# Optimization experiments

Measured on AMD Instinct MI355X. Metric: run time of the kernel, lower is better.

The kernel has to match this reference:

```python
import jax, jax.numpy as jnp
import numpy as np

B, N, F_IN, H, S = 8, 2048, 128, 128, 2
ALPHA = 0.1  # LeakyReLU slope


def setup_inputs() -> dict:
    key = jax.random.key(0)
    ks = jax.random.split(key, 10)
    X_bt = jax.random.normal(ks[0], (B, N, F_IN), dtype=jnp.float32)
    distance_matrix = jax.random.uniform(ks[1], (N, N), dtype=jnp.float32)
    sigmas = jnp.array([0.2, 1.0], dtype=jnp.float32)  # GaussianKernelGenerator scales[:2]
    # Per-scale GeoGATLayer params (stacked on leading scale dim)
    W_w = jax.random.normal(ks[2], (S, H, F_IN), dtype=jnp.float32) * (1.0 / np.sqrt(F_IN))
    W_b = jnp.zeros((S, H), dtype=jnp.float32)
    # attn_fc: Linear(2H, 1) split into the two halves acting on h_i and h_j
    a_i = jax.random.normal(ks[3], (S, H), dtype=jnp.float32) * (1.0 / np.sqrt(2 * H))
    a_j = jax.random.normal(ks[4], (S, H), dtype=jnp.float32) * (1.0 / np.sqrt(2 * H))
    a_b = jnp.zeros((S,), dtype=jnp.float32)
    thr = jnp.full((S,), 0.3, dtype=jnp.float32)
    fus_w = jax.random.normal(ks[5], (H, S * H), dtype=jnp.float32) * (1.0 / np.sqrt(S * H))
    fus_b = jnp.zeros((H,), dtype=jnp.float32)
    return {"X_bt": X_bt, "distance_matrix": distance_matrix, "sigmas": sigmas,
            "W_w": W_w, "W_b": W_b, "a_i": a_i, "a_j": a_j, "a_b": a_b,
            "thr": thr, "fus_w": fus_w, "fus_b": fus_b}


def _leaky_relu(x):
    return jnp.where(x >= 0, x, ALPHA * x)


def reference(X_bt, distance_matrix, sigmas, W_w, W_b, a_i, a_j, a_b, thr, fus_w, fus_b):
    n = distance_matrix.shape[0]
    # layer clones dist and sets diag=1.0 (only for the 1/d additive bias)
    dist_diag1 = distance_matrix.at[jnp.diag_indices(n)].set(1.0)
    inv_d = 1.0 / (dist_diag1 + 1e-5)  # (N,N)
    outs = []
    for s in range(S):
        h = jnp.einsum('bnf,hf->bnh', X_bt, W_w[s]) + W_b[s]  # (B,N,H)
        # attn_fc(cat(h_i,h_j)) == h_i@a_i + h_j@a_j + bias (no concat materialized)
        si = h @ a_i[s]  # (B,N)
        sj = h @ a_j[s]  # (B,N)
        e = _leaky_relu(si[:, :, None] + sj[:, None, :] + a_b[s])  # (B,N,N)
        e = e + inv_d[None]
        A = jnp.exp(-distance_matrix ** 2 / (2.0 * sigmas[s] ** 2))  # Gaussian kernel
        mask = jax.nn.sigmoid(10.0 * (A - thr[s]))
        e = e * mask[None]
        attn = jax.nn.softmax(e, axis=-1)  # dropout is identity in eval
        outs.append(jnp.einsum('bnm,bmh->bnh', attn, h))
    H_cat = jnp.concatenate(outs, axis=-1)  # (B,N,S*H)
    return jnp.einsum('bnk,hk->bnh', H_cat, fus_w) + fus_b
```

## Files before the change

### kernel.cpp

```cpp
#include <hip/hip_runtime.h>
#include <cstdint>
#include <cstddef>

#define BB 8
#define NN 2048
#define FF 128
#define HH 128
#define SS 2

typedef _Float16 f16x8 __attribute__((ext_vector_type(8)));
typedef _Float16 f16x4 __attribute__((ext_vector_type(4)));
typedef float f32x4 __attribute__((ext_vector_type(4)));

__global__ __launch_bounds__(256) void geo_kernel(
    const float* __restrict__ dist, const float* __restrict__ sigmas,
    const float* __restrict__ thr, _Float16* __restrict__ g1, float* __restrict__ g2)
{
    const size_t idx = ((size_t)blockIdx.x * 256 + threadIdx.x) * 8;
    const int s = (int)(idx >> 22);
    const int i = (int)((idx >> 11) & (NN - 1));
    const int j0 = (int)(idx & (NN - 1));
    const float sg = sigmas[s];
    const float inv2s2 = 1.0f / (2.0f * sg * sg);
    const float th = thr[s];
    const float* dp = dist + (size_t)i * NN + j0;
    float4 d0 = *(const float4*)dp, d1 = *(const float4*)(dp + 4);
    float dv[8] = {d0.x, d0.y, d0.z, d0.w, d1.x, d1.y, d1.z, d1.w};
    f16x8 o1; float og[8];
    #pragma unroll
    for (int k = 0; k < 8; ++k) {
        float d = dv[k];
        float A = __expf(-d * d * inv2s2);
        float msk = 1.0f / (1.0f + __expf(-10.0f * (A - th)));
        float dd = (j0 + k == i) ? 1.0f : d;
        float invd = 1.0f / (dd + 1e-5f);
        o1[k] = (_Float16)msk;
        og[k] = msk * invd;
    }
    *(f16x8*)(g1 + idx) = o1;
    *(float4*)(g2 + idx)     = (float4){og[0], og[1], og[2], og[3]};
    *(float4*)(g2 + idx + 4) = (float4){og[4], og[5], og[6], og[7]};
}

__global__ __launch_bounds__(256, 2) void prep_kernel(
    const float* __restrict__ X, const float* __restrict__ Ww, const float* __restrict__ Wb,
    const float* __restrict__ ai, const float* __restrict__ aj, const float* __restrict__ ab,
    _Float16* __restrict__ h_t, float* __restrict__ srow, float* __restrict__ scol)
{
    const int s = blockIdx.z, b = blockIdx.y;
    const int n0 = blockIdx.x * 64;
    const int tid = threadIdx.x;
    __shared__ __align__(16) unsigned char smem[51200];
    float* sredI = (float*)(smem + 49152);
    float* sredJ = (float*)(smem + 49152 + 1024);

    {
        const int r = tid >> 2, fq = tid & 3;
        const float* src = X + ((size_t)b * NN + n0 + r) * FF + fq * 32;
        unsigned char* dst = smem + r * 256;
        const unsigned rs = r & 15;
        #pragma unroll
        for (int k = 0; k < 4; ++k) {
            float4 v0 = *(const float4*)(src + k * 8);
            float4 v1 = *(const float4*)(src + k * 8 + 4);
            f16x8 h;
            h[0]=(_Float16)v0.x; h[1]=(_Float16)v0.y; h[2]=(_Float16)v0.z; h[3]=(_Float16)v0.w;
            h[4]=(_Float16)v1.x; h[5]=(_Float16)v1.y; h[6]=(_Float16)v1.z; h[7]=(_Float16)v1.w;
            *(f16x8*)(dst + (((fq * 4 + k) ^ rs) << 4)) = h;
        }
    }
    {
        const int ch = tid >> 1, kh8 = (tid & 1) * 8;
        const float* src = Ww + ((size_t)s * HH + ch) * FF + kh8 * 8;
        unsigned char* dst = smem + 16384 + ch * 256;
        const unsigned cs = ch & 15;
        #pragma unroll
        for (int k = 0; k < 8; ++k) {
            float4 v0 = *(const float4*)(src + k * 8);
            float4 v1 = *(const float4*)(src + k * 8 + 4);
            f16x8 h;
            h[0]=(_Float16)v0.x; h[1]=(_Float16)v0.y; h[2]=(_Float16)v0.z; h[3]=(_Float16)v0.w;
            h[4]=(_Float16)v1.x; h[5]=(_Float16)v1.y; h[6]=(_Float16)v1.z; h[7]=(_Float16)v1.w;
            *(f16x8*)(dst + (((kh8 + k) ^ cs) << 4)) = h;
        }
    }
    __syncthreads();

    const int wave = tid >> 6, lane = tid & 63;
    const int lm = lane & 15, lq = lane >> 4;
    f32x4 acc[4][2];
    #pragma unroll
    for (int m = 0; m < 4; ++m)
        #pragma unroll
        for (int n = 0; n < 2; ++n) acc[m][n] = (f32x4){0.f, 0.f, 0.f, 0.f};

    #pragma unroll
    for (int ks = 0; ks < 4; ++ks) {
        f16x8 af[4], bf[2];
        #pragma unroll
        for (int m = 0; m < 4; ++m) {
            int r = m * 16 + lm;
            af[m] = *(const f16x8*)(smem + r * 256 + ((((ks << 2) | lq) ^ (r & 15)) << 4));
        }
        #pragma unroll
        for (int n = 0; n < 2; ++n) {
            int ch = wave * 32 + n * 16 + lm;
            bf[n] = *(const f16x8*)(smem + 16384 + ch * 256 + ((((ks << 2) | lq) ^ (ch & 15)) << 4));
        }
        #pragma unroll
        for (int m = 0; m < 4; ++m)
            #pragma unroll
            for (int n = 0; n < 2; ++n)
                acc[m][n] = __builtin_amdgcn_mfma_f32_16x16x32_f16(af[m], bf[n], acc[m][n], 0, 0, 0);
    }

    const float wb0 = Wb[s * HH + wave * 32 + lm];
    const float wb1 = Wb[s * HH + wave * 32 + 16 + lm];
    const float ai0 = ai[s * HH + wave * 32 + lm];
    const float ai1 = ai[s * HH + wave * 32 + 16 + lm];
    const float aj0 = aj[s * HH + wave * 32 + lm];
    const float aj1 = aj[s * HH + wave * 32 + 16 + lm];
    float pI[4][4], pJ[4][4];
    #pragma unroll
    for (int m = 0; m < 4; ++m)
        #pragma unroll
        for (int r = 0; r < 4; ++r) {
            float h0 = acc[m][0][r] + wb0;
            float h1 = acc[m][1][r] + wb1;
            pI[m][r] = h0 * ai0 + h1 * ai1;
            pJ[m][r] = h0 * aj0 + h1 * aj1;
        }
    #pragma unroll
    for (int st = 1; st < 16; st <<= 1) {
        #pragma unroll
        for (int m = 0; m < 4; ++m)
            #pragma unroll
            for (int r = 0; r < 4; ++r) {
                pI[m][r] += __shfl_xor(pI[m][r], st);
                pJ[m][r] += __shfl_xor(pJ[m][r], st);
            }
    }
    __syncthreads();

    {
        #pragma unroll
        for (int m = 0; m < 4; ++m)
            #pragma unroll
            for (int n = 0; n < 2; ++n) {
                float wb = n ? wb1 : wb0;
                f16x4 hv;
                #pragma unroll
                for (int r = 0; r < 4; ++r) hv[r] = (_Float16)(acc[m][n][r] + wb);
                int ch = wave * 32 + n * 16 + lm;
                int slot = m * 2 + (lq >> 1);
                *(f16x4*)(smem + ch * 128 + ((slot ^ (ch & 7)) << 4) + (lq & 1) * 8) = hv;
            }
    }
    if (lm == 0) {
        #pragma unroll
        for (int m = 0; m < 4; ++m)
            #pragma unroll
            for (int r = 0; r < 4; ++r) {
                sredI[wave * 64 + m * 16 + lq * 4 + r] = pI[m][r];
                sredJ[wave * 64 + m * 16 + lq * 4 + r] = pJ[m][r];
            }
    }
    __syncthreads();
    {
        const int ch = tid >> 1, half = tid & 1;
        _Float16* dst = h_t + ((size_t)((s * BB + b) * HH + ch)) * NN + n0 + half * 32;
        const unsigned cs = ch & 7;
        #pragma unroll
        for (int k = 0; k < 4; ++k) {
            f16x8 v = *(const f16x8*)(smem + ch * 128 + (((half * 4 + k) ^ cs) << 4));
            *(f16x8*)(dst + k * 8) = v;
        }
    }
    if (tid < 64) {
        float sI = sredI[tid] + sredI[64 + tid] + sredI[128 + tid] + sredI[192 + tid] + ab[s];
        float sJ = sredJ[tid] + sredJ[64 + tid] + sredJ[128 + tid] + sredJ[192 + tid];
        size_t idx = (size_t)(s * BB + b) * NN + n0 + tid;
        srow[idx] = sI;
        scol[idx] = sJ;
    }
}

__global__ __launch_bounds__(512, 4) void attn_kernel(
    const _Float16* __restrict__ g1, const float* __restrict__ g2,
    const _Float16* __restrict__ h_t, const float* __restrict__ srow,
    const float* __restrict__ scol, _Float16* __restrict__ Hcat)
{
    __shared__ __align__(16) unsigned char smem[50176];
    float* scb  = (float*)(smem + 49152);
    float* lrow = (float*)(smem + 49664);

    const int bx = blockIdx.x;
    const int grp = bx & 7;
    const int i0 = (bx >> 3) * 64;
    const int s = grp >> 2;
    const int b0 = (grp & 3) * 2;

    const int tid = threadIdx.x;
    const int wave = tid >> 6, lane = tid & 63;
    const int lm = lane & 15, lq = lane >> 4;

    const int row = tid >> 3, jq = tid & 7;
    const int gi = i0 + row;
    const unsigned rsw = row & 7;
    const size_t sb0 = (size_t)(s * BB + b0) * NN;
    const size_t sb1 = sb0 + NN;
    const float si0 = srow[sb0 + gi];
    const float si1 = srow[sb1 + gi];
    const size_t girow = ((size_t)s * NN + gi) * NN;

    const int tb = tid >> 8, tch = (tid >> 1) & 127, tjh = tid & 1;
    const _Float16* hsrc = h_t + ((size_t)((s * BB + b0 + tb) * HH + tch)) * NN + tjh * 32;
    unsigned char* hdst = smem + 16384 + tb * 16384 + tch * 128;
    const unsigned hsw = tch & 7;

    const int wb = wave >> 2, cq = wave & 3;

    f32x4 acc[4][2];
    #pragma unroll
    for (int m = 0; m < 4; ++m)
        #pragma unroll
        for (int n = 0; n < 2; ++n) acc[m][n] = (f32x4){0.f, 0.f, 0.f, 0.f};
    float m0 = -3.0e38f, m1 = -3.0e38f, l0 = 0.f, l1 = 0.f;

    for (int jt = 0; jt < NN / 64; ++jt) {
        const int j0 = jt * 64;
        f16x8 hv0 = *(const f16x8*)(hsrc + j0);
        f16x8 hv1 = *(const f16x8*)(hsrc + j0 + 8);
        f16x8 hv2 = *(const f16x8*)(hsrc + j0 + 16);
        f16x8 hv3 = *(const f16x8*)(hsrc + j0 + 24);

        const int jb = j0 + jq * 8;
        f16x8 gv = *(const f16x8*)(g1 + girow + jb);
        float4 q0 = *(const float4*)(g2 + girow + jb);
        float4 q1 = *(const float4*)(g2 + girow + jb + 4);
        float4 c00 = *(const float4*)(scol + sb0 + jb);
        float4 c01 = *(const float4*)(scol + sb0 + jb + 4);
        float4 c10 = *(const float4*)(scol + sb1 + jb);
        float4 c11 = *(const float4*)(scol + sb1 + jb + 4);

        float e0[8], e1[8];
        #pragma unroll
        for (int k = 0; k < 8; ++k) {
            float gg = (k < 4) ? q0[k & 3] : q1[k & 3];
            float g1f = (float)gv[k];
            float t0 = si0 + ((k < 4) ? c00[k & 3] : c01[k & 3]);
            float t1 = si1 + ((k < 4) ? c10[k & 3] : c11[k & 3]);
            t0 = fmaxf(t0, 0.1f * t0);
            t1 = fmaxf(t1, 0.1f * t1);
            e0[k] = fmaf(t0, g1f, gg);
            e1[k] = fmaf(t1, g1f, gg);
        }
        float wm0 = fmaxf(fmaxf(fmaxf(e0[0], e0[1]), fmaxf(e0[2], e0[3])),
                          fmaxf(fmaxf(e0[4], e0[5]), fmaxf(e0[6], e0[7])));
        float wm1 = fmaxf(fmaxf(fmaxf(e1[0], e1[1]), fmaxf(e1[2], e1[3])),
                          fmaxf(fmaxf(e1[4], e1[5]), fmaxf(e1[6], e1[7])));
        #pragma unroll
        for (int st = 1; st < 8; st <<= 1) {
            wm0 = fmaxf(wm0, __shfl_xor(wm0, st));
            wm1 = fmaxf(wm1, __shfl_xor(wm1, st));
        }
        const float mn0 = fmaxf(m0, wm0), mn1 = fmaxf(m1, wm1);
        const float sc0 = __expf(m0 - mn0), sc1 = __expf(m1 - mn1);
        f16x8 pv0, pv1;
        float ps0 = 0.f, ps1 = 0.f;
        #pragma unroll
        for (int k = 0; k < 8; ++k) {
            float p0 = __expf(e0[k] - mn0); ps0 += p0; pv0[k] = (_Float16)p0;
            float p1 = __expf(e1[k] - mn1); ps1 += p1; pv1[k] = (_Float16)p1;
        }
        #pragma unroll
        for (int st = 1; st < 8; st <<= 1) {
            ps0 += __shfl_xor(ps0, st);
            ps1 += __shfl_xor(ps1, st);
        }
        l0 = l0 * sc0 + ps0; m0 = mn0;
        l1 = l1 * sc1 + ps1; m1 = mn1;
        {
            const unsigned off = row * 128 + ((jq ^ rsw) << 4);
            *(f16x8*)(smem + off) = pv0;
            *(f16x8*)(smem + 8192 + off) = pv1;
        }
        if (jq == 0) { scb[row] = sc0; scb[64 + row] = sc1; }

        *(f16x8*)(hdst + (((tjh * 4 + 0) ^ hsw) << 4)) = hv0;
        *(f16x8*)(hdst + (((tjh * 4 + 1) ^ hsw) << 4)) = hv1;
        *(f16x8*)(hdst + (((tjh * 4 + 2) ^ hsw) << 4)) = hv2;
        *(f16x8*)(hdst + (((tjh * 4 + 3) ^ hsw) << 4)) = hv3;
        __syncthreads();

        {
            const unsigned char* Pb = smem + wb * 8192;
            const unsigned char* Hb = smem + 16384 + wb * 16384;
            f16x8 bf[2][2];
            #pragma unroll
            for (int n = 0; n < 2; ++n) {
                const int ch = cq * 32 + n * 16 + lm;
                const unsigned cs = ch & 7;
                bf[n][0] = *(const f16x8*)(Hb + ch * 128 + ((lq ^ cs) << 4));
                bf[n][1] = *(const f16x8*)(Hb + ch * 128 + (((4 | lq) ^ cs) << 4));
            }
            #pragma unroll
            for (int mf = 0; mf < 4; ++mf) {
                const int r = mf * 16 + lm;
                const unsigned sw = r & 7;
                f16x8 a0 = *(const f16x8*)(Pb + r * 128 + ((lq ^ sw) << 4));
                f16x8 a1 = *(const f16x8*)(Pb + r * 128 + (((4 | lq) ^ sw) << 4));
                f32x4 scv = *(const f32x4*)(scb + wb * 64 + mf * 16 + lq * 4);
                #pragma unroll
                for (int n = 0; n < 2; ++n) {
                    acc[mf][n] *= scv;
                    acc[mf][n] = __builtin_amdgcn_mfma_f32_16x16x32_f16(a0, bf[n][0], acc[mf][n], 0, 0, 0);
                    acc[mf][n] = __builtin_amdgcn_mfma_f32_16x16x32_f16(a1, bf[n][1], acc[mf][n], 0, 0, 0);
                }
            }
        }
        __syncthreads();
    }

    if (jq == 0) { lrow[row] = l0; lrow[64 + row] = l1; }
    __syncthreads();

    _Float16* ebuf = (_Float16*)smem;
    #pragma unroll
    for (int mf = 0; mf < 4; ++mf) {
        f32x4 lv = *(const f32x4*)(lrow + wb * 64 + mf * 16 + lq * 4);
        f32x4 inv;
        #pragma unroll
        for (int r = 0; r < 4; ++r) {
            float x = lv[r];
            float iv = __builtin_amdgcn_rcpf(x);
            inv[r] = iv * (2.0f - x * iv);
        }
        #pragma unroll
        for (int n = 0; n < 2; ++n) {
            const int ecol = cq * 32 + n * 16 + lm;
            #pragma unroll
            for (int r = 0; r < 4; ++r)
                ebuf[wb * 8192 + (mf * 16 + lq * 4 + r) * 128 + ecol] =
                    (_Float16)(acc[mf][n][r] * inv[r]);
        }
    }
    __syncthreads();
    {
        const int eb = tid >> 8, er = (tid >> 2) & 63, eq = tid & 3;
        const _Float16* esrc = (const _Float16*)smem + eb * 8192 + er * 128 + eq * 32;
        _Float16* edst = Hcat + ((size_t)((b0 + eb) * NN + i0 + er)) * (SS * HH) + s * HH + eq * 32;
        #pragma unroll
        for (int k = 0; k < 4; ++k)
            *(f16x8*)(edst + k * 8) = *(const f16x8*)(esrc + k * 8);
    }
}

__global__ __launch_bounds__(256, 2) void fuse_kernel(
    const _Float16* __restrict__ Hcat, const float* __restrict__ fw,
    const float* __restrict__ fb, float* __restrict__ out)
{
    const int r0 = blockIdx.x * 32;
    const int tid = threadIdx.x;
    __shared__ __align__(16) unsigned char smem[49152];

    {
        const int r = tid >> 3, q = tid & 7;
        const _Float16* src = Hcat + (size_t)(r0 + r) * 256 + q * 32;
        unsigned char* dst = smem + r * 512;
        const unsigned rs = r & 7;
        #pragma unroll
        for (int k = 0; k < 4; ++k) {
            f16x8 v = *(const f16x8*)(src + k * 8);
            *(f16x8*)(dst + (((q * 4 + k) ^ rs) << 4)) = v;
        }
    }

    const int wave = tid >> 6, lane = tid & 63;
    const int lm = lane & 15, lq = lane >> 4;
    f32x4 acc[2][2];
    #pragma unroll
    for (int m = 0; m < 2; ++m)
        #pragma unroll
        for (int n = 0; n < 2; ++n) acc[m][n] = (f32x4){0.f, 0.f, 0.f, 0.f};

    for (int c = 0; c < 2; ++c) {
        __syncthreads();
        {
            const int ch = tid >> 1, kh8 = (tid & 1) * 8;
            const float* src = fw + (size_t)ch * 256 + c * 128 + kh8 * 8;
            unsigned char* dst = smem + 16384 + ch * 256;
            const unsigned cs = ch & 15;
            #pragma unroll
            for (int k = 0; k < 8; ++k) {
                float4 v0 = *(const float4*)(src + k * 8);
                float4 v1 = *(const float4*)(src + k * 8 + 4);
                f16x8 h;
                h[0]=(_Float16)v0.x; h[1]=(_Float16)v0.y; h[2]=(_Float16)v0.z; h[3]=(_Float16)v0.w;
                h[4]=(_Float16)v1.x; h[5]=(_Float16)v1.y; h[6]=(_Float16)v1.z; h[7]=(_Float16)v1.w;
                *(f16x8*)(dst + (((kh8 + k) ^ cs) << 4)) = h;
            }
        }
        __syncthreads();
        #pragma unroll
        for (int ks = 0; ks < 4; ++ks) {
            const int gks = c * 4 + ks;
            f16x8 af[2], bf[2];
            #pragma unroll
            for (int m = 0; m < 2; ++m) {
                int r = m * 16 + lm;
                af[m] = *(const f16x8*)(smem + r * 512 + ((((gks << 2) | lq) ^ (r & 7)) << 4));
            }
            #pragma unroll
            for (int n = 0; n < 2; ++n) {
                int ch = wave * 32 + n * 16 + lm;
                bf[n] = *(const f16x8*)(smem + 16384 + ch * 256 + ((((ks << 2) | lq) ^ (ch & 15)) << 4));
            }
            #pragma unroll
            for (int m = 0; m < 2; ++m)
                #pragma unroll
                for (int n = 0; n < 2; ++n)
                    acc[m][n] = __builtin_amdgcn_mfma_f32_16x16x32_f16(af[m], bf[n], acc[m][n], 0, 0, 0);
        }
    }
    {
        float fb0 = fb[wave * 32 + lm];
        float fb1 = fb[wave * 32 + 16 + lm];
        #pragma unroll
        for (int m = 0; m < 2; ++m)
            #pragma unroll
            for (int n = 0; n < 2; ++n) {
                float fbv = n ? fb1 : fb0;
                int ch = wave * 32 + n * 16 + lm;
                #pragma unroll
                for (int r = 0; r < 4; ++r)
                    out[(size_t)(r0 + m * 16 + lq * 4 + r) * HH + ch] = acc[m][n][r] + fbv;
            }
    }
}

extern "C" void kernel_launch(void* const* d_in, const int* in_sizes, int n_in,
                              void* d_out, int out_size, void* d_ws, size_t ws_size,
                              hipStream_t stream)
{
    const float* X      = (const float*)d_in[0];
    const float* dist   = (const float*)d_in[1];
    const float* sigmas = (const float*)d_in[2];
    const float* Ww     = (const float*)d_in[3];
    const float* Wb     = (const float*)d_in[4];
    const float* ai     = (const float*)d_in[5];
    const float* aj     = (const float*)d_in[6];
    const float* ab     = (const float*)d_in[7];
    const float* thr    = (const float*)d_in[8];
    const float* fw     = (const float*)d_in[9];
    const float* fb     = (const float*)d_in[10];
    float* out = (float*)d_out;

    char* ws = (char*)d_ws;
    float*     srow = (float*)(ws);
    float*     scol = (float*)(ws + 131072);
    _Float16*  h_t  = (_Float16*)(ws + 262144);
    _Float16*  Hcat = (_Float16*)(ws + 8650752);
    _Float16*  g1   = (_Float16*)(ws + 17039360);
    float*     g2   = (float*)(ws + 33816576);

    geo_kernel<<<(SS * NN * NN / 8) / 256, 256, 0, stream>>>(dist, sigmas, thr, g1, g2);
    prep_kernel<<<dim3(NN / 64, BB, SS), 256, 0, stream>>>(X, Ww, Wb, ai, aj, ab, h_t, srow, scol);
    attn_kernel<<<256, 512, 0, stream>>>(g1, g2, h_t, srow, scol, Hcat);
    fuse_kernel<<<BB * NN / 32, 256, 0, stream>>>(Hcat, fw, fb, out);
}
```

Measured before the change: 191.1 us.

## Double-buffer attention tiles and overlap MFMA with next tile's softmax

Restructures the attention main loop into a two-stage software pipeline. Global loads for the next 64-column tile are prefetched into registers, and the MFMA work for the previous tile is interleaved with the score/softmax phase of the current tile. P and H tiles are double-buffered in LDS, which cuts barriers to one per tile. This needs about 100KB of dynamic shared memory and more live registers, so the occupancy hint drops from 4 to 2 blocks. The aim is to hide global-load latency and expose MFMA/VALU overlap, at the cost of register pressure and possible spills.

```diff
diff --git a/kernel.cpp b/kernel.cpp
--- a/kernel.cpp
+++ b/kernel.cpp
@@ -185,14 +185,14 @@
     }
 }
 
-__global__ __launch_bounds__(512, 4) void attn_kernel(
+__global__ __launch_bounds__(512, 2) void attn_kernel(
     const _Float16* __restrict__ g1, const float* __restrict__ g2,
     const _Float16* __restrict__ h_t, const float* __restrict__ srow,
     const float* __restrict__ scol, _Float16* __restrict__ Hcat)
 {
-    __shared__ __align__(16) unsigned char smem[50176];
-    float* scb  = (float*)(smem + 49152);
-    float* lrow = (float*)(smem + 49664);
+    extern __shared__ __align__(16) unsigned char smem[];
+    float* scbf = (float*)(smem + 98304);
+    float* lrow = (float*)(smem + 99328);
 
     const int bx = blockIdx.x;
     const int grp = bx & 7;
@@ -215,7 +215,6 @@
 
     const int tb = tid >> 8, tch = (tid >> 1) & 127, tjh = tid & 1;
     const _Float16* hsrc = h_t + ((size_t)((s * BB + b0 + tb) * HH + tch)) * NN + tjh * 32;
-    unsigned char* hdst = smem + 16384 + tb * 16384 + tch * 128;
     const unsigned hsw = tch & 7;
 
     const int wb = wave >> 2, cq = wave & 3;
@@ -227,102 +226,121 @@
         for (int n = 0; n < 2; ++n) acc[m][n] = (f32x4){0.f, 0.f, 0.f, 0.f};
     float m0 = -3.0e38f, m1 = -3.0e38f, l0 = 0.f, l1 = 0.f;
 
-    for (int jt = 0; jt < NN / 64; ++jt) {
-        const int j0 = jt * 64;
-        f16x8 hv0 = *(const f16x8*)(hsrc + j0);
-        f16x8 hv1 = *(const f16x8*)(hsrc + j0 + 8);
-        f16x8 hv2 = *(const f16x8*)(hsrc + j0 + 16);
-        f16x8 hv3 = *(const f16x8*)(hsrc + j0 + 24);
-
-        const int jb = j0 + jq * 8;
-        f16x8 gv = *(const f16x8*)(g1 + girow + jb);
-        float4 q0 = *(const float4*)(g2 + girow + jb);
-        float4 q1 = *(const float4*)(g2 + girow + jb + 4);
-        float4 c00 = *(const float4*)(scol + sb0 + jb);
-        float4 c01 = *(const float4*)(scol + sb0 + jb + 4);
-        float4 c10 = *(const float4*)(scol + sb1 + jb);
-        float4 c11 = *(const float4*)(scol + sb1 + jb + 4);
-
-        float e0[8], e1[8];
-        #pragma unroll
-        for (int k = 0; k < 8; ++k) {
-            float gg = (k < 4) ? q0[k & 3] : q1[k & 3];
-            float g1f = (float)gv[k];
-            float t0 = si0 + ((k < 4) ? c00[k & 3] : c01[k & 3]);
-            float t1 = si1 + ((k < 4) ? c10[k & 3] : c11[k & 3]);
-            t0 = fmaxf(t0, 0.1f * t0);
-            t1 = fmaxf(t1, 0.1f * t1);
-            e0[k] = fmaf(t0, g1f, gg);
-            e1[k] = fmaf(t1, g1f, gg);
-        }
-        float wm0 = fmaxf(fmaxf(fmaxf(e0[0], e0[1]), fmaxf(e0[2], e0[3])),
-                          fmaxf(fmaxf(e0[4], e0[5]), fmaxf(e0[6], e0[7])));
-        float wm1 = fmaxf(fmaxf(fmaxf(e1[0], e1[1]), fmaxf(e1[2], e1[3])),
-                          fmaxf(fmaxf(e1[4], e1[5]), fmaxf(e1[6], e1[7])));
-        #pragma unroll
-        for (int st = 1; st < 8; st <<= 1) {
-            wm0 = fmaxf(wm0, __shfl_xor(wm0, st));
-            wm1 = fmaxf(wm1, __shfl_xor(wm1, st));
-        }
-        const float mn0 = fmaxf(m0, wm0), mn1 = fmaxf(m1, wm1);
-        const float sc0 = __expf(m0 - mn0), sc1 = __expf(m1 - mn1);
-        f16x8 pv0, pv1;
-        float ps0 = 0.f, ps1 = 0.f;
-        #pragma unroll
-        for (int k = 0; k < 8; ++k) {
-            float p0 = __expf(e0[k] - mn0); ps0 += p0; pv0[k] = (_Float16)p0;
-            float p1 = __expf(e1[k] - mn1); ps1 += p1; pv1[k] = (_Float16)p1;
-        }
-        #pragma unroll
-        for (int st = 1; st < 8; st <<= 1) {
-            ps0 += __shfl_xor(ps0, st);
-            ps1 += __shfl_xor(ps1, st);
-        }
-        l0 = l0 * sc0 + ps0; m0 = mn0;
-        l1 = l1 * sc1 + ps1; m1 = mn1;
-        {
-            const unsigned off = row * 128 + ((jq ^ rsw) << 4);
-            *(f16x8*)(smem + off) = pv0;
-            *(f16x8*)(smem + 8192 + off) = pv1;
-        }
-        if (jq == 0) { scb[row] = sc0; scb[64 + row] = sc1; }
-
-        *(f16x8*)(hdst + (((tjh * 4 + 0) ^ hsw) << 4)) = hv0;
-        *(f16x8*)(hdst + (((tjh * 4 + 1) ^ hsw) << 4)) = hv1;
-        *(f16x8*)(hdst + (((tjh * 4 + 2) ^ hsw) << 4)) = hv2;
-        *(f16x8*)(hdst + (((tjh * 4 + 3) ^ hsw) << 4)) = hv3;
+    f16x8 gA, gB, hA0, hA1, hA2, hA3, hB0, hB1, hB2, hB3;
+    float4 qA0, qA1, qB0, qB1;
+    float4 cA00, cA01, cA10, cA11, cB00, cB01, cB10, cB11;
+
+#define LOADG(G, Q0, Q1, C00, C01, C10, C11, H0, H1, H2, H3, J0) {            \
+    const int jb_ = (J0) + jq * 8;                                            \
+    G  = *(const f16x8*)(g1 + girow + jb_);                                   \
+    Q0 = *(const float4*)(g2 + girow + jb_);                                  \
+    Q1 = *(const float4*)(g2 + girow + jb_ + 4);                              \
+    C00 = *(const float4*)(scol + sb0 + jb_);                                 \
+    C01 = *(const float4*)(scol + sb0 + jb_ + 4);                             \
+    C10 = *(const float4*)(scol + sb1 + jb_);                                 \
+    C11 = *(const float4*)(scol + sb1 + jb_ + 4);                             \
+    H0 = *(const f16x8*)(hsrc + (J0));                                        \
+    H1 = *(const f16x8*)(hsrc + (J0) + 8);                                    \
+    H2 = *(const f16x8*)(hsrc + (J0) + 16);                                   \
+    H3 = *(const f16x8*)(hsrc + (J0) + 24);                                   \
+}
+
+#define PHASE1(G, Q0, Q1, C00, C01, C10, C11, H0, H1, H2, H3, PB) {           \
+    float e0[8], e1[8];                                                       \
+    _Pragma("unroll")                                                         \
+    for (int k = 0; k < 8; ++k) {                                             \
+        float gg = (k < 4) ? Q0[k & 3] : Q1[k & 3];                           \
+        float g1f = (float)G[k];                                              \
+        float t0 = si0 + ((k < 4) ? C00[k & 3] : C01[k & 3]);                 \
+        float t1 = si1 + ((k < 4) ? C10[k & 3] : C11[k & 3]);                 \
+        t0 = fmaxf(t0, 0.1f * t0);                                            \
+        t1 = fmaxf(t1, 0.1f * t1);                                            \
+        e0[k] = fmaf(t0, g1f, gg);                                            \
+        e1[k] = fmaf(t1, g1f, gg);                                            \
+    }                                                                         \
+    float wm0 = fmaxf(fmaxf(fmaxf(e0[0], e0[1]), fmaxf(e0[2], e0[3])),        \
+                      fmaxf(fmaxf(e0[4], e0[5]), fmaxf(e0[6], e0[7])));       \
+    float wm1 = fmaxf(fmaxf(fmaxf(e1[0], e1[1]), fmaxf(e1[2], e1[3])),        \
+                      fmaxf(fmaxf(e1[4], e1[5]), fmaxf(e1[6], e1[7])));       \
+    _Pragma("unroll")                                                         \
+    for (int st = 1; st < 8; st <<= 1) {                                      \
+        wm0 = fmaxf(wm0, __shfl_xor(wm0, st));                                \
+        wm1 = fmaxf(wm1, __shfl_xor(wm1, st));                                \
+    }                                                                         \
+    const float mn0 = fmaxf(m0, wm0), mn1 = fmaxf(m1, wm1);                   \
+    const float sc0 = __expf(m0 - mn0), sc1 = __expf(m1 - mn1);               \
+    f16x8 pv0, pv1;                                                           \
+    float ps0 = 0.f, ps1 = 0.f;                                               \
+    _Pragma("unroll")                                                         \
+    for (int k = 0; k < 8; ++k) {                                             \
+        float p0 = __expf(e0[k] - mn0); ps0 += p0; pv0[k] = (_Float16)p0;     \
+        float p1 = __expf(e1[k] - mn1); ps1 += p1; pv1[k] = (_Float16)p1;     \
+    }                                                                         \
+    _Pragma("unroll")                                                         \
+    for (int st = 1; st < 8; st <<= 1) {                                      \
+        ps0 += __shfl_xor(ps0, st);                                           \
+        ps1 += __shfl_xor(ps1, st);                                           \
+    }                                                                         \
+    l0 = l0 * sc0 + ps0; m0 = mn0;                                            \
+    l1 = l1 * sc1 + ps1; m1 = mn1;                                            \
+    {                                                                         \
+        unsigned char* Pd = smem + (PB) * 16384;                              \
+        const unsigned off = row * 128 + ((jq ^ rsw) << 4);                   \
+        *(f16x8*)(Pd + off) = pv0;                                            \
+        *(f16x8*)(Pd + 8192 + off) = pv1;                                     \
+    }                                                                         \
+    if (jq == 0) { scbf[(PB) * 128 + row] = sc0;                              \
+                   scbf[(PB) * 128 + 64 + row] = sc1; }                       \
+    {                                                                         \
+        unsigned char* hd = smem + 32768 + (PB) * 32768 + tb * 16384 + tch * 128; \
+        *(f16x8*)(hd + (((tjh * 4 + 0) ^ hsw) << 4)) = H0;                    \
+        *(f16x8*)(hd + (((tjh * 4 + 1) ^ hsw) << 4)) = H1;                    \
+        *(f16x8*)(hd + (((tjh * 4 + 2) ^ hsw) << 4)) = H2;                    \
+        *(f16x8*)(hd + (((tjh * 4 + 3) ^ hsw) << 4)) = H3;                    \
+    }                                                                         \
+}
+
+#define MFMA_STEP(MB) {                                                       \
+    const unsigned char* Pb = smem + (MB) * 16384 + wb * 8192;                \
+    const unsigned char* Hb = smem + 32768 + (MB) * 32768 + wb * 16384;       \
+    f16x8 bf[2][2];                                                           \
+    _Pragma("unroll")                                                         \
+    for (int n = 0; n < 2; ++n) {                                             \
+        const int ch = cq * 32 + n * 16 + lm;                                 \
+        const unsigned cs = ch & 7;                                           \
+        bf[n][0] = *(const f16x8*)(Hb + ch * 128 + ((lq ^ cs) << 4));         \
+        bf[n][1] = *(const f16x8*)(Hb + ch * 128 + (((4 | lq) ^ cs) << 4));   \
+    }                                                                         \
+    _Pragma("unroll")                                                         \
+    for (int mf = 0; mf < 4; ++mf) {                                          \
+        const int r = mf * 16 + lm;                                           \
+        const unsigned sw = r & 7;                                            \
+        f16x8 a0 = *(const f16x8*)(Pb + r * 128 + ((lq ^ sw) << 4));          \
+        f16x8 a1 = *(const f16x8*)(Pb + r * 128 + (((4 | lq) ^ sw) << 4));    \
+        f32x4 scv = *(const f32x4*)(scbf + (MB) * 128 + wb * 64 + mf * 16 + lq * 4); \
+        _Pragma("unroll")                                                     \
+        for (int n = 0; n < 2; ++n) {                                         \
+            acc[mf][n] *= scv;                                                \
+            acc[mf][n] = __builtin_amdgcn_mfma_f32_16x16x32_f16(a0, bf[n][0], acc[mf][n], 0, 0, 0); \
+            acc[mf][n] = __builtin_amdgcn_mfma_f32_16x16x32_f16(a1, bf[n][1], acc[mf][n], 0, 0, 0); \
+        }                                                                     \
+    }                                                                         \
+}
+
+    LOADG(gA, qA0, qA1, cA00, cA01, cA10, cA11, hA0, hA1, hA2, hA3, 0);
+    for (int jt = 0; jt < 32; jt += 2) {
+        LOADG(gB, qB0, qB1, cB00, cB01, cB10, cB11, hB0, hB1, hB2, hB3, (jt + 1) * 64);
+        if (jt > 0) MFMA_STEP(1);
+        PHASE1(gA, qA0, qA1, cA00, cA01, cA10, cA11, hA0, hA1, hA2, hA3, 0);
         __syncthreads();
-
-        {
-            const unsigned char* Pb = smem + wb * 8192;
-            const unsigned char* Hb = smem + 16384 + wb * 16384;
-            f16x8 bf[2][2];
-            #pragma unroll
-            for (int n = 0; n < 2; ++n) {
-                const int ch = cq * 32 + n * 16 + lm;
-                const unsigned cs = ch & 7;
-                bf[n][0] = *(const f16x8*)(Hb + ch * 128 + ((lq ^ cs) << 4));
-                bf[n][1] = *(const f16x8*)(Hb + ch * 128 + (((4 | lq) ^ cs) << 4));
-            }
-            #pragma unroll
-            for (int mf = 0; mf < 4; ++mf) {
-                const int r = mf * 16 + lm;
-                const unsigned sw = r & 7;
-                f16x8 a0 = *(const f16x8*)(Pb + r * 128 + ((lq ^ sw) << 4));
-                f16x8 a1 = *(const f16x8*)(Pb + r * 128 + (((4 | lq) ^ sw) << 4));
-                f32x4 scv = *(const f32x4*)(scb + wb * 64 + mf * 16 + lq * 4);
-                #pragma unroll
-                for (int n = 0; n < 2; ++n) {
-                    acc[mf][n] *= scv;
-                    acc[mf][n] = __builtin_amdgcn_mfma_f32_16x16x32_f16(a0, bf[n][0], acc[mf][n], 0, 0, 0);
-                    acc[mf][n] = __builtin_amdgcn_mfma_f32_16x16x32_f16(a1, bf[n][1], acc[mf][n], 0, 0, 0);
-                }
-            }
-        }
+        if (jt + 2 < 32)
+            LOADG(gA, qA0, qA1, cA00, cA01, cA10, cA11, hA0, hA1, hA2, hA3, (jt + 2) * 64);
+        MFMA_STEP(0);
+        PHASE1(gB, qB0, qB1, cB00, cB01, cB10, cB11, hB0, hB1, hB2, hB3, 1);
         __syncthreads();
     }
-
     if (jq == 0) { lrow[row] = l0; lrow[64 + row] = l1; }
+    MFMA_STEP(1);
     __syncthreads();
 
     _Float16* ebuf = (_Float16*)smem;
@@ -354,6 +372,9 @@
         for (int k = 0; k < 4; ++k)
             *(f16x8*)(edst + k * 8) = *(const f16x8*)(esrc + k * 8);
     }
+#undef LOADG
+#undef PHASE1
+#undef MFMA_STEP
 }
 
 __global__ __launch_bounds__(256, 2) void fuse_kernel(
@@ -466,6 +487,6 @@
 
     geo_kernel<<<(SS * NN * NN / 8) / 256, 256, 0, stream>>>(dist, sigmas, thr, g1, g2);
     prep_kernel<<<dim3(NN / 64, BB, SS), 256, 0, stream>>>(X, Ww, Wb, ai, aj, ab, h_t, srow, scol);
-    attn_kernel<<<256, 512, 0, stream>>>(g1, g2, h_t, srow, scol, Hcat);
+    attn_kernel<<<256, 512, 99840, stream>>>(g1, g2, h_t, srow, scol, Hcat);
     fuse_kernel<<<BB * NN / 32, 256, 0, stream>>>(Hcat, fw, fb, out);
 }
```

Measured after the change: 181.2 us. -5.2%, faster.
